# Kernel tuning notes

Measured on AMD Instinct MI355X. Metric: run time of the kernel, lower is better.

The kernel has to match this reference:

```python
import jax, jax.numpy as jnp
import numpy as np

PI = 3.141592653589793
TAU = 2.0      # tau for both rpe_lif (spikingjelly default 2.0) and act_conv (params['tau'])
V_TH = 1.0     # spikingjelly LIFNode default v_threshold
EPS = 1e-5     # LayerNorm / BatchNorm eps


@jax.custom_vjp
def atan_spike(x):
    # Heaviside forward, ATan surrogate backward (spikingjelly surrogate.ATan, alpha=2)
    return (x >= 0.0).astype(x.dtype)

def _atan_fwd(x):
    return atan_spike(x), x

def _atan_bwd(x, g):
    # (alpha/2) / (1 + ((pi/2)*alpha*x)^2) with alpha=2 -> 1/(1+(pi*x)^2)
    return (g / (1.0 + (PI * x) ** 2),)

atan_spike.defvjp(_atan_fwd, _atan_bwd)


def lif(x_seq, tau=TAU):
    """Multi-step LIF: decay_input=True, v_reset=0, hard reset, detach_reset.
    x_seq: [T, ...]; returns spikes [T, ...]."""
    def step(v, x):
        v = v + (x - v) / tau                      # neuronal charge
        s = atan_spike(v - V_TH)                   # fire
        v = v * (1.0 - jax.lax.stop_gradient(s))   # detached hard reset to 0
        return v, s
    _, spikes = jax.lax.scan(step, jnp.zeros_like(x_seq[0]), x_seq)
    return spikes


def setup_inputs() -> dict:
    key = jax.random.key(0)
    ks = jax.random.split(key, 8)
    B, L, D, T = 256, 50, 128, 4
    n_items, n_h, n_v = 100001, 8, 4
    emb = jax.random.normal(ks[0], (n_items, D), jnp.float32) * 0.5
    emb = emb.at[0].set(0.0)  # padding_idx=0
    return {
        "item_seq": jax.random.randint(ks[1], (B, L), 0, n_items, jnp.int32),
        "emb_table": emb,
        "ln_gamma": jnp.ones((D,), jnp.float32),
        "ln_beta": jnp.zeros((D,), jnp.float32),
        "conv_v_w": jax.random.normal(ks[2], (n_v, L), jnp.float32) * float(1.0 / np.sqrt(L)),
        # per-length kernels stored padded: kernel for length k=i+1 is conv_h_w[i, :, :k, :]
        "conv_h_w": jax.random.normal(ks[3], (L, n_h, L, D), jnp.float32) * 0.02,
        "bn_gamma": jnp.ones((L, n_h), jnp.float32),
        "bn_beta": jnp.zeros((L, n_h), jnp.float32),
        "fc_h_w": jax.random.normal(ks[4], (D, n_h * L), jnp.float32) * 0.05,
        "fc_h_b": jnp.zeros((D,), jnp.float32),
        "fc_v_w": jax.random.normal(ks[5], (D, n_v * D), jnp.float32) * 0.04,
        "fc_v_b": jnp.zeros((D,), jnp.float32),
        "T": 4,
    }


def reference(item_seq, emb_table, ln_gamma, ln_beta, conv_v_w, conv_h_w,
              bn_gamma, bn_beta, fc_h_w, fc_h_b, fc_v_w, fc_v_b, T):
    B, L = item_seq.shape
    D = emb_table.shape[1]
    n_h = conv_h_w.shape[1]
    n_v = conv_v_w.shape[0]

    # embedding + LayerNorm
    emb = emb_table[item_seq]                                   # [B,L,D]
    mu = emb.mean(-1, keepdims=True)
    var = emb.var(-1, keepdims=True)
    x = (emb - mu) / jnp.sqrt(var + EPS) * ln_gamma + ln_beta   # [B,L,D]

    # repeat over T and spike (rpe_lif)
    s = lif(jnp.broadcast_to(x, (T, B, L, D)))                  # binary spikes [T,B,L,D]

    # vertical conv: kernel (L,1), no bias -> collapses seq axis
    out_v = jnp.einsum('tbld,cl->tbcd', s, conv_v_w).reshape(T, B, n_v * D)

    # horizontal multi-scale convs + BN(train stats) + LIF + global max pool
    s2 = s.reshape(T * B, 1, L, D)
    pools = []
    for i in range(L):
        k = i + 1
        w = conv_h_w[i, :, :k, :][:, None]                      # [n_h,1,k,D]
        y = jax.lax.conv_general_dilated(
            s2, w, (1, 1), 'VALID',
            dimension_numbers=('NCHW', 'OIHW', 'NCHW'))[:, :, :, 0]  # [TB,n_h,L-k+1]
        m = y.mean(axis=(0, 2))                                  # BN over (T*B, spatial)
        v = y.var(axis=(0, 2))
        y = (y - m[:, None]) * (bn_gamma[i][:, None] / jnp.sqrt(v[:, None] + EPS)) + bn_beta[i][:, None]
        y = lif(y.reshape(T, B, n_h, L - k + 1))                 # [T,B,n_h,L-k+1]
        pools.append(y.max(axis=-1))                             # [T,B,n_h]
    out_h = jnp.concatenate(pools, axis=-1)                      # [T,B,n_h*L]

    out_h = (out_h @ fc_h_w.T + fc_h_b).mean(0)                  # [B,D]
    out_v = out_v.mean(0) @ fc_v_w.T + fc_v_b                    # [B,D]
    return out_h + out_v
```

## Files before the change

### kernel.cpp

```cpp
#include <hip/hip_runtime.h>

#define B_ 256
#define L_ 50
#define D_ 128
#define T_ 4
#define NH 8
#define NV 4
#define TB_ (T_*B_)
#define EPSF 1e-5f

typedef _Float16 h8 __attribute__((ext_vector_type(8)));
typedef float f4 __attribute__((ext_vector_type(4)));

__device__ __forceinline__ float waveSum(float v) {
    #pragma unroll
    for (int o = 32; o > 0; o >>= 1) v += __shfl_down(v, o, 64);
    return v;
}

__device__ __forceinline__ size_t yoff(int i) {
    return (size_t)8192 * (size_t)(50 * i - (i * (i - 1)) / 2);
}

__global__ __launch_bounds__(256) void k0_wsplit(
        const float* __restrict__ w, _Float16* __restrict__ whl) {
    int dk = blockIdx.x, i = blockIdx.y;
    int t = threadIdx.x;
    int c = t >> 4, gd = t & 15;
    int h = c & 7;
    bool live = (i < 50) && (dk <= i);
    const float* src = w + (((size_t)i * NH + h) * L_ + dk) * D_ + gd * 8;
    h8 o;
    #pragma unroll
    for (int e = 0; e < 8; ++e) {
        float wv = live ? src[e] : 0.f;
        _Float16 hi = (_Float16)wv;
        o[e] = (c < 8) ? hi : (_Float16)((wv - (float)hi) * 1024.f);
    }
    *(h8*)(whl + (((size_t)i * 50 + dk) * 16 + c) * 128 + ((gd ^ c) & 15) * 8) = o;
}

__global__ __launch_bounds__(128) void k1_embed_ln_lif(
        const int* __restrict__ item, const float* __restrict__ tab,
        const float* __restrict__ g, const float* __restrict__ be,
        _Float16* __restrict__ s16, float* __restrict__ smean) {
    int bid = blockIdx.x;
    int b = bid / L_, l = bid % L_;
    int d = threadIdx.x;
    int wid = d >> 6, lane = d & 63;
    __shared__ float red[2];
    int it = item[b * L_ + l];
    float e = tab[(size_t)it * D_ + d];
    float sm_ = waveSum(e);
    if (lane == 0) red[wid] = sm_;
    __syncthreads();
    float mu = (red[0] + red[1]) * (1.f / 128.f);
    __syncthreads();
    float df = e - mu;
    float s2 = waveSum(df * df);
    if (lane == 0) red[wid] = s2;
    __syncthreads();
    float var = (red[0] + red[1]) * (1.f / 128.f);
    float x = df / sqrtf(var + EPSF) * g[d] + be[d];
    float v = 0.f, acc = 0.f;
    int pos = (((d >> 3) ^ l) & 15) * 8 + (d & 7);
    #pragma unroll
    for (int t = 0; t < T_; ++t) {
        v += (x - v) * 0.5f;
        float sp = (v >= 1.f) ? 1.f : 0.f;
        v *= (1.f - sp);
        s16[((size_t)(t * B_ + b) * L_ + l) * D_ + pos] = (_Float16)sp;
        acc += sp;
    }
    smean[((size_t)b * L_ + l) * D_ + d] = acc * 0.25f;
}

template<int MTG>
__global__ __launch_bounds__(512, 4) void k2x(
        const _Float16* __restrict__ s16, const _Float16* __restrict__ whl,
        float* __restrict__ y, int mode) {
    extern __shared__ __align__(16) char lds[];
    const int tbq = blockIdx.x;
    int grp, joff;
    if (mode == 0) {
        if (blockIdx.y < 2) { grp = 0; joff = 2 * blockIdx.y; }
        else { grp = blockIdx.y - 1; joff = 0; }
    } else {
        if (blockIdx.y < 4) { grp = blockIdx.y + 1; joff = 2; }
        else { grp = blockIdx.y + 5; joff = 0; }
    }
    const int i0 = grp * 4;
    const int kmax = (i0 + 4 <= 50) ? (i0 + 4) : 50;
    const int tid = threadIdx.x;
    const int wave = tid >> 6, lane = tid & 63;
    const int tq = wave >> 2;
    const int dc = wave & 3;
    const int c_ = lane & 15, g = lane >> 4;

    {
        const float4* src = (const float4*)(s16 + (size_t)tbq * 4 * (L_ * D_));
        float4* dst = (float4*)lds;
        for (int idx = tid; idx < 3200; idx += 512) dst[idx] = src[idx];
    }

    const int boffc = c_ * 256 + ((((dc << 2) + g) ^ c_) & 15) * 16;
    const char* gB = (const char*)whl + (size_t)i0 * 204800 + boffc;

    h8 bf0 = *(const h8*)(gB);
    h8 bf1 = *(const h8*)(gB + 204800);
    h8 bf2 = *(const h8*)(gB + 409600);
    h8 bf3 = *(const h8*)(gB + 614400);
    __syncthreads();

    f4 acc[4][2][MTG];
    #pragma unroll
    for (int sc = 0; sc < 4; ++sc)
        #pragma unroll
        for (int tt = 0; tt < 2; ++tt)
            #pragma unroll
            for (int jt = 0; jt < MTG; ++jt) { f4 z = {0.f, 0.f, 0.f, 0.f}; acc[sc][tt][jt] = z; }

    for (int dk = 0; dk < kmax; ++dk) {
        const bool more = (dk + 1 < kmax);
        h8 bn0, bn1, bn2, bn3;
        if (more) {
            const char* p = gB + (size_t)(dk + 1) * 4096;
            bn0 = *(const h8*)(p);
            bn1 = *(const h8*)(p + 204800);
            bn2 = *(const h8*)(p + 409600);
            bn3 = *(const h8*)(p + 614400);
        }
        #pragma unroll
        for (int tt = 0; tt < 2; ++tt) {
            const int tbL = tq * 2 + tt;
            #pragma unroll
            for (int jt = 0; jt < MTG; ++jt) {
                int l = (joff + jt) * 16 + c_ + dk; if (l > 49) l = 49;
                h8 a = *(const h8*)(lds + tbL * 12800 + l * 256 +
                                    ((((dc << 2) + g) ^ l) & 15) * 16);
                acc[0][tt][jt] = __builtin_amdgcn_mfma_f32_16x16x32_f16(a, bf0, acc[0][tt][jt], 0, 0, 0);
                acc[1][tt][jt] = __builtin_amdgcn_mfma_f32_16x16x32_f16(a, bf1, acc[1][tt][jt], 0, 0, 0);
                acc[2][tt][jt] = __builtin_amdgcn_mfma_f32_16x16x32_f16(a, bf2, acc[2][tt][jt], 0, 0, 0);
                acc[3][tt][jt] = __builtin_amdgcn_mfma_f32_16x16x32_f16(a, bf3, acc[3][tt][jt], 0, 0, 0);
            }
        }
        bf0 = bn0; bf1 = bn1; bf2 = bn2; bf3 = bn3;
    }

    f4* mbuf = (f4*)lds;
    #pragma unroll
    for (int jt = 0; jt < MTG; ++jt) {
        __syncthreads();
        if (dc != 0) {
            f4* wp = mbuf + (size_t)(((dc - 1) * 2 + tq) * 8) * 64 + lane;
            #pragma unroll
            for (int sc = 0; sc < 4; ++sc)
                #pragma unroll
                for (int tt = 0; tt < 2; ++tt)
                    wp[(sc * 2 + tt) * 64] = acc[sc][tt][jt];
        }
        __syncthreads();
        if (dc == 0) {
            #pragma unroll
            for (int dd = 0; dd < 3; ++dd) {
                const f4* rp = mbuf + (size_t)((dd * 2 + tq) * 8) * 64 + lane;
                #pragma unroll
                for (int sc = 0; sc < 4; ++sc)
                    #pragma unroll
                    for (int tt = 0; tt < 2; ++tt)
                        acc[sc][tt][jt] += rp[(sc * 2 + tt) * 64];
            }
        }
    }

    if (dc == 0) {
        const bool hiLane = (c_ < 8);
        const int h = c_ & 7;
        #pragma unroll
        for (int sc = 0; sc < 4; ++sc) {
            const int i = i0 + sc;
            const int J = 50 - i;
            if (J <= 0) continue;
            #pragma unroll
            for (int tt = 0; tt < 2; ++tt) {
                const int tb = tbq * 4 + tq * 2 + tt;
                size_t yb = yoff(i) + ((size_t)tb * NH + h) * J;
                #pragma unroll
                for (int jt = 0; jt < MTG; ++jt) {
                    #pragma unroll
                    for (int r = 0; r < 4; ++r) {
                        float lo = __shfl_xor(acc[sc][tt][jt][r], 8, 64);
                        int j = (joff + jt) * 16 + g * 4 + r;
                        if (hiLane && j < J) y[yb + j] = acc[sc][tt][jt][r] + lo * (1.f / 1024.f);
                    }
                }
            }
        }
    }
}

__global__ __launch_bounds__(256) void k3_partial(
        const float* __restrict__ y, float* __restrict__ psum) {
    int ih = blockIdx.x, ck = blockIdx.y;
    int i = ih >> 3, h = ih & 7;
    int J = 50 - i;
    size_t yb = yoff(i);
    int tid = threadIdx.x;
    int grp = tid >> 5, sub = tid & 31;
    float sm = 0.f, ss = 0.f;
    for (int tb = ck * 128 + grp; tb < (ck + 1) * 128; tb += 8) {
        const float* row = y + yb + ((size_t)tb * NH + h) * J;
        for (int j = sub; j < J; j += 32) { float v = row[j]; sm += v; ss += v * v; }
    }
    __shared__ float r1[4], r2[4];
    float a = waveSum(sm), b = waveSum(ss);
    int wid = tid >> 6, lane = tid & 63;
    if (lane == 0) { r1[wid] = a; r2[wid] = b; }
    __syncthreads();
    if (tid == 0) {
        psum[((size_t)ih * 8 + ck) * 2]     = r1[0] + r1[1] + r1[2] + r1[3];
        psum[((size_t)ih * 8 + ck) * 2 + 1] = r2[0] + r2[1] + r2[2] + r2[3];
    }
}

__global__ __launch_bounds__(256) void k3_final(
        const float* __restrict__ psum, const float* __restrict__ bng,
        float* __restrict__ statm, float* __restrict__ stats_) {
    int ih = blockIdx.x * 256 + threadIdx.x;
    if (ih >= 400) return;
    float S = 0.f, Q = 0.f;
    for (int ck = 0; ck < 8; ++ck) {
        S += psum[((size_t)ih * 8 + ck) * 2];
        Q += psum[((size_t)ih * 8 + ck) * 2 + 1];
    }
    int i = ih >> 3;
    float cnt = 1024.f * (float)(50 - i);
    float m = S / cnt;
    float var = Q / cnt - m * m; if (var < 0.f) var = 0.f;
    statm[ih] = m;
    stats_[ih] = bng[ih] / sqrtf(var + EPSF);
}

__global__ __launch_bounds__(512) void k4_bn_lif_pool(
        const float* __restrict__ y, const float* __restrict__ statm,
        const float* __restrict__ stats_, const float* __restrict__ bnb,
        float* __restrict__ ps) {
    int b = blockIdx.x, i = blockIdx.y, J = L_ - i;
    int h = threadIdx.x >> 6, lane = threadIdx.x & 63;
    int ih = i * NH + h;
    float m = statm[ih], sc = stats_[ih], bb = bnb[ih];
    size_t yb = yoff(i);
    bool valid = lane < J;
    float v = 0.f; int cnt = 0;
    #pragma unroll
    for (int t = 0; t < T_; ++t) {
        int tb = t * B_ + b;
        float yn;
        if (valid) {
            float raw = y[yb + ((size_t)tb * NH + h) * J + lane];
            yn = (raw - m) * sc + bb;
        } else yn = -1e30f;
        v += (yn - v) * 0.5f;
        bool sp = (v >= 1.f);
        if (sp) v = 0.f;
        if (__any(sp)) cnt++;
    }
    if (lane == 0) ps[(size_t)b * 400 + ih] = (float)cnt;
}

__global__ __launch_bounds__(128) void k5_final(
        const float* __restrict__ smean, const float* __restrict__ ps,
        const float* __restrict__ convv, const float* __restrict__ fchw,
        const float* __restrict__ fchb, const float* __restrict__ fcvw,
        const float* __restrict__ fcvb, float* __restrict__ out) {
    __shared__ float sm_l[L_ * D_];
    __shared__ float vm[NV * D_];
    __shared__ float ps_l[400];
    int b = blockIdx.x, tid = threadIdx.x;
    for (int idx = tid; idx < L_ * D_; idx += 128) sm_l[idx] = smean[(size_t)b * (L_ * D_) + idx];
    for (int idx = tid; idx < 400; idx += 128) ps_l[idx] = ps[(size_t)b * 400 + idx];
    __syncthreads();
    int d = tid;
    #pragma unroll
    for (int c = 0; c < NV; ++c) {
        float a = 0.f;
        for (int l = 0; l < L_; ++l) a += convv[c * L_ + l] * sm_l[l * D_ + d];
        vm[c * D_ + d] = a;
    }
    __syncthreads();
    float acc = fchb[d] + fcvb[d];
    float ah = 0.f;
    for (int ih = 0; ih < 400; ++ih) ah += ps_l[ih] * fchw[d * 400 + ih];
    acc += ah * 0.25f;
    float av = 0.f;
    for (int cd = 0; cd < NV * D_; ++cd) av += vm[cd] * fcvw[d * (NV * D_) + cd];
    acc += av;
    out[(size_t)b * D_ + d] = acc;
}

extern "C" void kernel_launch(void* const* d_in, const int* in_sizes, int n_in,
                              void* d_out, int out_size, void* d_ws, size_t ws_size,
                              hipStream_t stream) {
    const int*   item  = (const int*)d_in[0];
    const float* tab   = (const float*)d_in[1];
    const float* lng   = (const float*)d_in[2];
    const float* lnb   = (const float*)d_in[3];
    const float* convv = (const float*)d_in[4];
    const float* convh = (const float*)d_in[5];
    const float* bng   = (const float*)d_in[6];
    const float* bnb   = (const float*)d_in[7];
    const float* fchw  = (const float*)d_in[8];
    const float* fchb  = (const float*)d_in[9];
    const float* fcvw  = (const float*)d_in[10];
    const float* fcvb  = (const float*)d_in[11];
    float* out = (float*)d_out;

    char* ws = (char*)d_ws;
    _Float16* s16  = (_Float16*)(ws);
    float* smean   = (float*)(ws + 13107200LL);
    float* y       = (float*)(ws + 19660800LL);
    _Float16* whl  = (_Float16*)(ws + 61440000LL);
    float* statm   = (float*)(ws + 72089600LL);
    float* stats_  = (float*)(ws + 72091200LL);
    float* ps      = (float*)(ws + 72092800LL);
    float* psum    = (float*)(ws + 72502400LL);

    k0_wsplit<<<dim3(50, 52), 256, 0, stream>>>(convh, whl);
    k1_embed_ln_lif<<<B_ * L_, 128, 0, stream>>>(item, tab, lng, lnb, s16, smean);
    k2x<2><<<dim3(256, 10), 512, 51200, stream>>>(s16, whl, y, 0);
    k2x<1><<<dim3(256, 8), 512, 51200, stream>>>(s16, whl, y, 1);
    k3_partial<<<dim3(400, 8), 256, 0, stream>>>(y, psum);
    k3_final<<<dim3(2, 1), 256, 0, stream>>>(psum, bng, statm, stats_);
    k4_bn_lif_pool<<<dim3(B_, L_), 512, 0, stream>>>(y, statm, stats_, bnb, ps);
    k5_final<<<B_, 128, 0, stream>>>(smean, ps, convv, fchw, fchb, fcvw, fcvb, out);
}
```

Baseline: 311.6 us.

## Merge conv MFMA launches into one persistent kernel with balanced job lists

Replaces the two k2x launches (4608 blocks that each reload the spike tile into LDS) with a single k2m launch of 512 blocks. Each block loads its 4-sample spike tile once and then walks a static job table of (group, j-offset, tile count) entries, chosen so the two job lists carry roughly equal MFMA work. The cross-wave reduction now uses a separate LDS region, split into two halves to keep it small, and the MFMA loop is wrapped in s_setprio. The risks are much lower parallelism (only 512 blocks on a 256-CU part), longer serial jobs per block, and a larger LDS footprint that limits occupancy.

Measured after the change: 303.4 us. 1.03x faster.

```diff
diff --git a/kernel.cpp b/kernel.cpp
--- a/kernel.cpp
+++ b/kernel.cpp
@@ -75,34 +75,24 @@
     smean[((size_t)b * L_ + l) * D_ + d] = acc * 0.25f;
 }
 
+
+__device__ const int JT_N[2] = {6, 12};
+__device__ const int JT_i0[2][12] = {
+    {48, 32, 28, 24, 20, 0,  0, 0, 0, 0, 0, 0},
+    {16, 16, 12, 12, 8, 8, 4, 4, 36, 40, 44, 0}};
+__device__ const int JT_jo[2][12] = {
+    {0, 0, 0, 0, 0, 0,  0, 0, 0, 0, 0, 0},
+    {0, 2, 0, 2, 0, 2, 0, 2, 0, 0, 0, 2}};
+__device__ const int JT_mt[2][12] = {
+    {1, 2, 2, 2, 2, 2,  0, 0, 0, 0, 0, 0},
+    {2, 1, 2, 1, 2, 1, 2, 1, 1, 1, 1, 2}};
+
 template<int MTG>
-__global__ __launch_bounds__(512, 4) void k2x(
-        const _Float16* __restrict__ s16, const _Float16* __restrict__ whl,
-        float* __restrict__ y, int mode) {
-    extern __shared__ __align__(16) char lds[];
-    const int tbq = blockIdx.x;
-    int grp, joff;
-    if (mode == 0) {
-        if (blockIdx.y < 2) { grp = 0; joff = 2 * blockIdx.y; }
-        else { grp = blockIdx.y - 1; joff = 0; }
-    } else {
-        if (blockIdx.y < 4) { grp = blockIdx.y + 1; joff = 2; }
-        else { grp = blockIdx.y + 5; joff = 0; }
-    }
-    const int i0 = grp * 4;
+__device__ __forceinline__ void k2m_job(
+        const char* lds, char* mrg, const _Float16* __restrict__ whl,
+        float* __restrict__ y, int i0, int joff,
+        int tbq, int tq, int dc, int c_, int g) {
     const int kmax = (i0 + 4 <= 50) ? (i0 + 4) : 50;
-    const int tid = threadIdx.x;
-    const int wave = tid >> 6, lane = tid & 63;
-    const int tq = wave >> 2;
-    const int dc = wave & 3;
-    const int c_ = lane & 15, g = lane >> 4;
-
-    {
-        const float4* src = (const float4*)(s16 + (size_t)tbq * 4 * (L_ * D_));
-        float4* dst = (float4*)lds;
-        for (int idx = tid; idx < 3200; idx += 512) dst[idx] = src[idx];
-    }
-
     const int boffc = c_ * 256 + ((((dc << 2) + g) ^ c_) & 15) * 16;
     const char* gB = (const char*)whl + (size_t)i0 * 204800 + boffc;
 
@@ -110,7 +100,6 @@
     h8 bf1 = *(const h8*)(gB + 204800);
     h8 bf2 = *(const h8*)(gB + 409600);
     h8 bf3 = *(const h8*)(gB + 614400);
-    __syncthreads();
 
     f4 acc[4][2][MTG];
     #pragma unroll
@@ -130,6 +119,7 @@
             bn2 = *(const h8*)(p + 409600);
             bn3 = *(const h8*)(p + 614400);
         }
+        __builtin_amdgcn_s_setprio(1);
         #pragma unroll
         for (int tt = 0; tt < 2; ++tt) {
             const int tbL = tq * 2 + tt;
@@ -144,31 +134,36 @@
                 acc[3][tt][jt] = __builtin_amdgcn_mfma_f32_16x16x32_f16(a, bf3, acc[3][tt][jt], 0, 0, 0);
             }
         }
+        __builtin_amdgcn_s_setprio(0);
         bf0 = bn0; bf1 = bn1; bf2 = bn2; bf3 = bn3;
     }
 
-    f4* mbuf = (f4*)lds;
+    f4* mbuf = (f4*)mrg;
+    const int lane = (threadIdx.x & 63);
     #pragma unroll
     for (int jt = 0; jt < MTG; ++jt) {
-        __syncthreads();
-        if (dc != 0) {
-            f4* wp = mbuf + (size_t)(((dc - 1) * 2 + tq) * 8) * 64 + lane;
-            #pragma unroll
-            for (int sc = 0; sc < 4; ++sc)
+        #pragma unroll
+        for (int sp = 0; sp < 2; ++sp) {
+            __syncthreads();
+            if (dc != 0) {
+                f4* wp = mbuf + (size_t)(((dc - 1) * 2 + tq) * 4) * 64 + lane;
                 #pragma unroll
-                for (int tt = 0; tt < 2; ++tt)
-                    wp[(sc * 2 + tt) * 64] = acc[sc][tt][jt];
-        }
-        __syncthreads();
-        if (dc == 0) {
-            #pragma unroll
-            for (int dd = 0; dd < 3; ++dd) {
-                const f4* rp = mbuf + (size_t)((dd * 2 + tq) * 8) * 64 + lane;
-                #pragma unroll
-                for (int sc = 0; sc < 4; ++sc)
+                for (int scl = 0; scl < 2; ++scl)
                     #pragma unroll
                     for (int tt = 0; tt < 2; ++tt)
-                        acc[sc][tt][jt] += rp[(sc * 2 + tt) * 64];
+                        wp[(scl * 2 + tt) * 64] = acc[sp * 2 + scl][tt][jt];
+            }
+            __syncthreads();
+            if (dc == 0) {
+                #pragma unroll
+                for (int dd = 0; dd < 3; ++dd) {
+                    const f4* rp = mbuf + (size_t)((dd * 2 + tq) * 4) * 64 + lane;
+                    #pragma unroll
+                    for (int scl = 0; scl < 2; ++scl)
+                        #pragma unroll
+                        for (int tt = 0; tt < 2; ++tt)
+                            acc[sp * 2 + scl][tt][jt] += rp[(scl * 2 + tt) * 64];
+                }
             }
         }
     }
@@ -199,6 +194,37 @@
     }
 }
 
+__global__ __launch_bounds__(512, 4) void k2m(
+        const _Float16* __restrict__ s16, const _Float16* __restrict__ whl,
+        float* __restrict__ y) {
+    extern __shared__ __align__(16) char lds[];
+    char* mrg = lds + 51200;
+    const int tbq = blockIdx.x;
+    const int sg = blockIdx.y;
+    const int tid = threadIdx.x;
+    const int wave = tid >> 6, lane = tid & 63;
+    const int tq = wave >> 2;
+    const int dc = wave & 3;
+    const int c_ = lane & 15, g = lane >> 4;
+
+    {
+        const float4* src = (const float4*)(s16 + (size_t)tbq * 4 * (L_ * D_));
+        float4* dst = (float4*)lds;
+        for (int idx = tid; idx < 3200; idx += 512) dst[idx] = src[idx];
+    }
+    __syncthreads();
+
+    const int nj = JT_N[sg];
+    for (int jo = 0; jo < nj; ++jo) {
+        const int i0 = JT_i0[sg][jo];
+        const int joff = JT_jo[sg][jo];
+        if (JT_mt[sg][jo] == 2)
+            k2m_job<2>(lds, mrg, whl, y, i0, joff, tbq, tq, dc, c_, g);
+        else
+            k2m_job<1>(lds, mrg, whl, y, i0, joff, tbq, tq, dc, c_, g);
+    }
+}
+
 __global__ __launch_bounds__(256) void k3_partial(
         const float* __restrict__ y, float* __restrict__ psum) {
     int ih = blockIdx.x, ck = blockIdx.y;
@@ -325,10 +351,12 @@
     float* ps      = (float*)(ws + 72092800LL);
     float* psum    = (float*)(ws + 72502400LL);
 
+    hipFuncSetAttribute(reinterpret_cast<const void*>(&k2m),
+        hipFuncAttributeMaxDynamicSharedMemorySize, 75776);
+
     k0_wsplit<<<dim3(50, 52), 256, 0, stream>>>(convh, whl);
     k1_embed_ln_lif<<<B_ * L_, 128, 0, stream>>>(item, tab, lng, lnb, s16, smean);
-    k2x<2><<<dim3(256, 10), 512, 51200, stream>>>(s16, whl, y, 0);
-    k2x<1><<<dim3(256, 8), 512, 51200, stream>>>(s16, whl, y, 1);
+    k2m<<<dim3(256, 2), 512, 75776, stream>>>(s16, whl, y);
     k3_partial<<<dim3(400, 8), 256, 0, stream>>>(y, psum);
     k3_final<<<dim3(2, 1), 256, 0, stream>>>(psum, bng, statm, stats_);
     k4_bn_lif_pool<<<dim3(B_, L_), 512, 0, stream>>>(y, statm, stats_, bnb, ps);
```
